# Kernel tuning notes

Hardware: AMD Instinct MI355X
Metric: run time of the kernel (lower is better)

Reference implementation:

```python
import jax, jax.numpy as jnp
import numpy as np

GAMMA = 0.5  # RBF bandwidth, matches init_kwargs gamma


def setup_inputs() -> dict:
    key = jax.random.key(0)
    x = jax.random.normal(key, (8192, 64), dtype=jnp.float32)
    return {"x": x}


def reference(x):
    # Gram[i, j] = exp(-gamma * ||x_i - x_j||^2), computed fully batched.
    # ||xi - xj||^2 = ||xi||^2 + ||xj||^2 - 2 <xi, xj>
    sq = jnp.sum(x * x, axis=-1)                      # [n]
    d2 = sq[:, None] + sq[None, :] - 2.0 * (x @ x.T)  # [n, n]
    d2 = jnp.maximum(d2, 0.0)                         # numerical floor
    out = jnp.exp(-GAMMA * d2)                        # [n, n]
    n = x.shape[0]
    return out.reshape(n, -1)
```

## Files before the change

### kernel.cpp

```cpp
#include <hip/hip_runtime.h>


#define GAMMA 0.5f

typedef __attribute__((ext_vector_type(8))) _Float16 half8;
typedef __attribute__((ext_vector_type(4))) float f32x4;

__global__ __launch_bounds__(256) void quant_kernel(const float* __restrict__ x,
                                                    unsigned short* __restrict__ H,
                                                    float* __restrict__ sq) {
    int tid = blockIdx.x * 256 + threadIdx.x;
    int row = tid >> 4, c4 = tid & 15;
    float4 v = ((const float4*)x)[tid];
    float e[4] = {v.x, v.y, v.z, v.w};
    unsigned short hb[4];
    float s = 0.f;
    #pragma unroll
    for (int i = 0; i < 4; ++i) {
        _Float16 h = (_Float16)e[i];
        float hf = (float)h;
        s = fmaf(hf, hf, s);
        hb[i] = __builtin_bit_cast(unsigned short, h);
    }
    int rr = row & 127;
    size_t base = (size_t)(row >> 7) * 16384;
    int b = (rr * 128 + c4 * 8) ^ ((rr & 7) << 4);
    uint2 hw = {(unsigned)hb[0] | ((unsigned)hb[1] << 16),
                (unsigned)hb[2] | ((unsigned)hb[3] << 16)};
    *(uint2*)((char*)H + base + b) = hw;
    s += __shfl_xor(s, 1); s += __shfl_xor(s, 2);
    s += __shfl_xor(s, 4); s += __shfl_xor(s, 8);
    if (c4 == 0) sq[row] = s;
}

__global__ __launch_bounds__(256, 4) void rbf_mfma7(const unsigned short* __restrict__ H,
                                                    const float* __restrict__ sq,
                                                    float* __restrict__ out, int N) {
    __shared__ unsigned short Ah[8192], Bh[8192];

    const int tid = threadIdx.x;
    const int i0 = blockIdx.y * 128, j0 = blockIdx.x * 128;
    const int w = tid >> 6, lane = tid & 63;
    const int fr = lane & 15, kg = lane >> 4;
    const int wr = (w >> 1) * 64, wc = (w & 1) * 64;

    {
        const uint4* ga = (const uint4*)(H + (size_t)i0 * 64);
        const uint4* gb = (const uint4*)(H + (size_t)j0 * 64);
        #pragma unroll
        for (int t = 0; t < 4; ++t) {
            ((uint4*)Ah)[t * 256 + tid] = ga[t * 256 + tid];
            ((uint4*)Bh)[t * 256 + tid] = gb[t * 256 + tid];
        }
    }
    __syncthreads();

    f32x4 acc[4][4];
    #pragma unroll
    for (int p = 0; p < 4; ++p)
        #pragma unroll
        for (int q = 0; q < 4; ++q) acc[p][q] = (f32x4)(0.f);

    #pragma unroll
    for (int ks = 0; ks < 2; ++ks) {
        const int kb = ks * 64 + kg * 16;
        half8 ah[4], bh[4];
        #pragma unroll
        for (int p = 0; p < 4; ++p) {
            int R = wr + p * 16 + fr;
            int off = (R * 128 + kb) ^ ((R & 7) << 4);
            ah[p] = *(const half8*)((const char*)Ah + off);
        }
        #pragma unroll
        for (int q = 0; q < 4; ++q) {
            int R = wc + q * 16 + fr;
            int off = (R * 128 + kb) ^ ((R & 7) << 4);
            bh[q] = *(const half8*)((const char*)Bh + off);
        }
        #pragma unroll
        for (int p = 0; p < 4; ++p)
            #pragma unroll
            for (int q = 0; q < 4; ++q)
                acc[p][q] = __builtin_amdgcn_mfma_f32_16x16x32_f16(bh[q], ah[p], acc[p][q], 0, 0, 0);
    }

    #pragma unroll
    for (int p = 0; p < 4; ++p) {
        int ri = wr + p * 16 + fr;
        float sa = sq[i0 + ri];
        float* rowp = out + (size_t)(i0 + ri) * N + j0;
        #pragma unroll
        for (int q = 0; q < 4; ++q) {
            int c = wc + q * 16 + kg * 4;
            float4 sb = *(const float4*)&sq[j0 + c];
            f32x4 a = acc[p][q];
            float4 r;
            r.x = __expf(-GAMMA * fmaxf(fmaf(-2.f, a[0], sa + sb.x), 0.f));
            r.y = __expf(-GAMMA * fmaxf(fmaf(-2.f, a[1], sa + sb.y), 0.f));
            r.z = __expf(-GAMMA * fmaxf(fmaf(-2.f, a[2], sa + sb.z), 0.f));
            r.w = __expf(-GAMMA * fmaxf(fmaf(-2.f, a[3], sa + sb.w), 0.f));
            *(float4*)(rowp + c) = r;
        }
    }
}

extern "C" void kernel_launch(void* const* d_in, const int* in_sizes, int n_in,
                              void* d_out, int out_size, void* d_ws, size_t ws_size,
                              hipStream_t stream) {
    (void)n_in; (void)ws_size; (void)out_size;
    const float* x = (const float*)d_in[0];
    float* out = (float*)d_out;
    const int K = 64;
    const int N = in_sizes[0] / K;

    unsigned short* H = (unsigned short*)d_ws;
    float* sq = (float*)(H + (size_t)N * K);

    quant_kernel<<<dim3(N * K / 4 / 256), dim3(256), 0, stream>>>(x, H, sq);
    rbf_mfma7<<<dim3(N / 128, N / 128), dim3(256), 0, stream>>>(H, sq, out, N);
}
```

Measured before the change: 61.66 us.

## Process four column tiles per block with register-prefetched B tiles

Each block now covers four consecutive 128-column tiles. The A tile stays resident in shared memory, and the next B tile is loaded into registers while the current tile's exp epilogue and stores run. This cuts the grid size, avoids reloading A and reduces block launch overhead, and aims to overlap global loads with output writes. In exchange it adds two block barriers per tile, raises register pressure from the prefetch buffers, and leaves fewer blocks to spread across CUs.

Result: slower. 78.09 us (+26.6%).

```diff
diff --git a/kernel.cpp b/kernel.cpp
--- a/kernel.cpp
+++ b/kernel.cpp
@@ -2,6 +2,7 @@
 
 
 #define GAMMA 0.5f
+#define TJ 4
 
 typedef __attribute__((ext_vector_type(8))) _Float16 half8;
 typedef __attribute__((ext_vector_type(4))) float f32x4;
@@ -33,20 +34,21 @@
     if (c4 == 0) sq[row] = s;
 }
 
-__global__ __launch_bounds__(256, 4) void rbf_mfma7(const unsigned short* __restrict__ H,
+__global__ __launch_bounds__(256, 4) void rbf_mfma8(const unsigned short* __restrict__ H,
                                                     const float* __restrict__ sq,
                                                     float* __restrict__ out, int N) {
     __shared__ unsigned short Ah[8192], Bh[8192];
 
     const int tid = threadIdx.x;
-    const int i0 = blockIdx.y * 128, j0 = blockIdx.x * 128;
+    const int i0 = blockIdx.y * 128;
+    const int j0b = blockIdx.x * (128 * TJ);
     const int w = tid >> 6, lane = tid & 63;
     const int fr = lane & 15, kg = lane >> 4;
     const int wr = (w >> 1) * 64, wc = (w & 1) * 64;
 
     {
         const uint4* ga = (const uint4*)(H + (size_t)i0 * 64);
-        const uint4* gb = (const uint4*)(H + (size_t)j0 * 64);
+        const uint4* gb = (const uint4*)(H + (size_t)j0b * 64);
         #pragma unroll
         for (int t = 0; t < 4; ++t) {
             ((uint4*)Ah)[t * 256 + tid] = ga[t * 256 + tid];
@@ -55,51 +57,76 @@
     }
     __syncthreads();
 
-    f32x4 acc[4][4];
-    #pragma unroll
-    for (int p = 0; p < 4; ++p)
-        #pragma unroll
-        for (int q = 0; q < 4; ++q) acc[p][q] = (f32x4)(0.f);
+    for (int tj = 0; tj < TJ; ++tj) {
+        const int j0 = j0b + tj * 128;
 
-    #pragma unroll
-    for (int ks = 0; ks < 2; ++ks) {
-        const int kb = ks * 64 + kg * 16;
-        half8 ah[4], bh[4];
-        #pragma unroll
-        for (int p = 0; p < 4; ++p) {
-            int R = wr + p * 16 + fr;
-            int off = (R * 128 + kb) ^ ((R & 7) << 4);
-            ah[p] = *(const half8*)((const char*)Ah + off);
-        }
-        #pragma unroll
-        for (int q = 0; q < 4; ++q) {
-            int R = wc + q * 16 + fr;
-            int off = (R * 128 + kb) ^ ((R & 7) << 4);
-            bh[q] = *(const half8*)((const char*)Bh + off);
-        }
+        f32x4 acc[4][4];
         #pragma unroll
         for (int p = 0; p < 4; ++p)
             #pragma unroll
-            for (int q = 0; q < 4; ++q)
-                acc[p][q] = __builtin_amdgcn_mfma_f32_16x16x32_f16(bh[q], ah[p], acc[p][q], 0, 0, 0);
-    }
+            for (int q = 0; q < 4; ++q) acc[p][q] = (f32x4)(0.f);
 
-    #pragma unroll
-    for (int p = 0; p < 4; ++p) {
-        int ri = wr + p * 16 + fr;
-        float sa = sq[i0 + ri];
-        float* rowp = out + (size_t)(i0 + ri) * N + j0;
         #pragma unroll
-        for (int q = 0; q < 4; ++q) {
-            int c = wc + q * 16 + kg * 4;
-            float4 sb = *(const float4*)&sq[j0 + c];
-            f32x4 a = acc[p][q];
-            float4 r;
-            r.x = __expf(-GAMMA * fmaxf(fmaf(-2.f, a[0], sa + sb.x), 0.f));
-            r.y = __expf(-GAMMA * fmaxf(fmaf(-2.f, a[1], sa + sb.y), 0.f));
-            r.z = __expf(-GAMMA * fmaxf(fmaf(-2.f, a[2], sa + sb.z), 0.f));
-            r.w = __expf(-GAMMA * fmaxf(fmaf(-2.f, a[3], sa + sb.w), 0.f));
-            *(float4*)(rowp + c) = r;
+        for (int ks = 0; ks < 2; ++ks) {
+            const int kb = ks * 64 + kg * 16;
+            half8 ah[4], bh[4];
+            #pragma unroll
+            for (int p = 0; p < 4; ++p) {
+                int R = wr + p * 16 + fr;
+                int off = (R * 128 + kb) ^ ((R & 7) << 4);
+                ah[p] = *(const half8*)((const char*)Ah + off);
+            }
+            #pragma unroll
+            for (int q = 0; q < 4; ++q) {
+                int R = wc + q * 16 + fr;
+                int off = (R * 128 + kb) ^ ((R & 7) << 4);
+                bh[q] = *(const half8*)((const char*)Bh + off);
+            }
+            #pragma unroll
+            for (int p = 0; p < 4; ++p)
+                #pragma unroll
+                for (int q = 0; q < 4; ++q)
+                    acc[p][q] = __builtin_amdgcn_mfma_f32_16x16x32_f16(bh[q], ah[p], acc[p][q], 0, 0, 0);
+        }
+
+        uint4 pb[4];
+        if (tj + 1 < TJ) {
+            const uint4* gb = (const uint4*)(H + (size_t)(j0 + 128) * 64);
+            #pragma unroll
+            for (int t = 0; t < 4; ++t) pb[t] = gb[t * 256 + tid];
+        }
+
+        #pragma unroll
+        for (int p = 0; p < 4; ++p) {
+            int ri = wr + p * 16 + fr;
+            float sa = sq[i0 + ri];
+            float* rowp = out + (size_t)(i0 + ri) * N + j0;
+            #pragma unroll
+            for (int q = 0; q < 4; ++q) {
+                int c = wc + q * 16 + kg * 4;
+                float4 sb = *(const float4*)&sq[j0 + c];
+                f32x4 a = acc[p][q];
+                float4 r;
+                r.x = __expf(-GAMMA * fmaxf(fmaf(-2.f, a[0], sa + sb.x), 0.f));
+                r.y = __expf(-GAMMA * fmaxf(fmaf(-2.f, a[1], sa + sb.y), 0.f));
+                r.z = __expf(-GAMMA * fmaxf(fmaf(-2.f, a[2], sa + sb.z), 0.f));
+                r.w = __expf(-GAMMA * fmaxf(fmaf(-2.f, a[3], sa + sb.w), 0.f));
+                *(float4*)(rowp + c) = r;
+            }
+        }
+
+        if (tj + 1 < TJ) {
+            asm volatile("s_waitcnt lgkmcnt(0)" ::: "memory");
+            __builtin_amdgcn_sched_barrier(0);
+            __builtin_amdgcn_s_barrier();
+            __builtin_amdgcn_sched_barrier(0);
+            #pragma unroll
+            for (int t = 0; t < 4; ++t)
+                ((uint4*)Bh)[t * 256 + tid] = pb[t];
+            asm volatile("s_waitcnt lgkmcnt(0)" ::: "memory");
+            __builtin_amdgcn_sched_barrier(0);
+            __builtin_amdgcn_s_barrier();
+            __builtin_amdgcn_sched_barrier(0);
         }
     }
 }
@@ -117,5 +144,5 @@
     float* sq = (float*)(H + (size_t)N * K);
 
     quant_kernel<<<dim3(N * K / 4 / 256), dim3(256), 0, stream>>>(x, H, sq);
-    rbf_mfma7<<<dim3(N / 128, N / 128), dim3(256), 0, stream>>>(H, sq, out, N);
+    rbf_mfma8<<<dim3(N / (128 * TJ), N / 128), dim3(256), 0, stream>>>(H, sq, out, N);
 }
```

## Stage output tiles through LDS for full-row coalesced stores, remap warps to row strips

Applied to the files above, without the earlier changes.

Each warp now owns a 32x128 strip (2x8 MFMA tiles) instead of a 64x64 quadrant. After the exp epilogue, results go through a swizzled per-warp LDS buffer that reuses the operand shared memory. They are then written as 512-byte contiguous row segments, so each wave writes two full rows per store. This targets poor write coalescing on the 256MB output, which dominates runtime, at the cost of an extra LDS round trip and a block barrier.

Measured after the change: 54.24 us, median of 2. 12.0% less time.

```diff
diff --git a/kernel.cpp b/kernel.cpp
--- a/kernel.cpp
+++ b/kernel.cpp
@@ -33,16 +33,18 @@
     if (c4 == 0) sq[row] = s;
 }
 
-__global__ __launch_bounds__(256, 4) void rbf_mfma7(const unsigned short* __restrict__ H,
-                                                    const float* __restrict__ sq,
-                                                    float* __restrict__ out, int N) {
-    __shared__ unsigned short Ah[8192], Bh[8192];
+__global__ __launch_bounds__(256, 4) void rbf_mfma10(const unsigned short* __restrict__ H,
+                                                     const float* __restrict__ sq,
+                                                     float* __restrict__ out, int N) {
+    __shared__ __align__(16) char smem[32768];
+    unsigned short* Ah = (unsigned short*)smem;
+    unsigned short* Bh = (unsigned short*)(smem + 16384);
 
     const int tid = threadIdx.x;
     const int i0 = blockIdx.y * 128, j0 = blockIdx.x * 128;
     const int w = tid >> 6, lane = tid & 63;
     const int fr = lane & 15, kg = lane >> 4;
-    const int wr = (w >> 1) * 64, wc = (w & 1) * 64;
+    const int wr = w * 32;
 
     {
         const uint4* ga = (const uint4*)(H + (size_t)i0 * 64);
@@ -55,43 +57,44 @@
     }
     __syncthreads();
 
-    f32x4 acc[4][4];
+    f32x4 acc[2][8];
     #pragma unroll
-    for (int p = 0; p < 4; ++p)
+    for (int p = 0; p < 2; ++p)
         #pragma unroll
-        for (int q = 0; q < 4; ++q) acc[p][q] = (f32x4)(0.f);
+        for (int q = 0; q < 8; ++q) acc[p][q] = (f32x4)(0.f);
 
     #pragma unroll
     for (int ks = 0; ks < 2; ++ks) {
         const int kb = ks * 64 + kg * 16;
-        half8 ah[4], bh[4];
+        half8 ah[2], bh[8];
         #pragma unroll
-        for (int p = 0; p < 4; ++p) {
+        for (int p = 0; p < 2; ++p) {
             int R = wr + p * 16 + fr;
             int off = (R * 128 + kb) ^ ((R & 7) << 4);
             ah[p] = *(const half8*)((const char*)Ah + off);
         }
         #pragma unroll
-        for (int q = 0; q < 4; ++q) {
-            int R = wc + q * 16 + fr;
+        for (int q = 0; q < 8; ++q) {
+            int R = q * 16 + fr;
             int off = (R * 128 + kb) ^ ((R & 7) << 4);
             bh[q] = *(const half8*)((const char*)Bh + off);
         }
         #pragma unroll
-        for (int p = 0; p < 4; ++p)
+        for (int p = 0; p < 2; ++p)
             #pragma unroll
-            for (int q = 0; q < 4; ++q)
+            for (int q = 0; q < 8; ++q)
                 acc[p][q] = __builtin_amdgcn_mfma_f32_16x16x32_f16(bh[q], ah[p], acc[p][q], 0, 0, 0);
     }
 
+    __syncthreads();
+    float* wbuf = (float*)smem + w * 2048;
+
     #pragma unroll
-    for (int p = 0; p < 4; ++p) {
-        int ri = wr + p * 16 + fr;
-        float sa = sq[i0 + ri];
-        float* rowp = out + (size_t)(i0 + ri) * N + j0;
+    for (int p = 0; p < 2; ++p) {
+        float sa = sq[i0 + wr + p * 16 + fr];
         #pragma unroll
-        for (int q = 0; q < 4; ++q) {
-            int c = wc + q * 16 + kg * 4;
+        for (int q = 0; q < 8; ++q) {
+            int c = q * 16 + kg * 4;
             float4 sb = *(const float4*)&sq[j0 + c];
             f32x4 a = acc[p][q];
             float4 r;
@@ -99,7 +102,15 @@
             r.y = __expf(-GAMMA * fmaxf(fmaf(-2.f, a[1], sa + sb.y), 0.f));
             r.z = __expf(-GAMMA * fmaxf(fmaf(-2.f, a[2], sa + sb.z), 0.f));
             r.w = __expf(-GAMMA * fmaxf(fmaf(-2.f, a[3], sa + sb.w), 0.f));
-            *(float4*)(rowp + c) = r;
+            *(float4*)&wbuf[fr * 128 + (c ^ ((fr & 7) << 2))] = r;
+        }
+        const int half = lane >> 5, lc = lane & 31;
+        #pragma unroll
+        for (int i = 0; i < 8; ++i) {
+            int rl = i * 2 + half;
+            float4 v = *(const float4*)&wbuf[rl * 128 + ((lc * 4) ^ ((rl & 7) << 2))];
+            int grow = i0 + wr + p * 16 + rl;
+            *(float4*)(out + (size_t)grow * N + j0 + lc * 4) = v;
         }
     }
 }
@@ -117,5 +128,5 @@
     float* sq = (float*)(H + (size_t)N * K);
 
     quant_kernel<<<dim3(N * K / 4 / 256), dim3(256), 0, stream>>>(x, H, sq);
-    rbf_mfma7<<<dim3(N / 128, N / 128), dim3(256), 0, stream>>>(H, sq, out, N);
+    rbf_mfma10<<<dim3(N / 128, N / 128), dim3(256), 0, stream>>>(H, sq, out, N);
 }
```
